# Performance work log

Hardware: AMD Instinct MI355X
Metric: run time of the kernel (lower is better)

## Reference

```python
import jax, jax.numpy as jnp
import numpy as np

HEADS = 16
HEAD_DIM = 64
DIM = 1024
INNER = HEADS * HEAD_DIM
EPS = 1e-5


def setup_inputs() -> dict:
    key = jax.random.key(0)
    k_x, k_qkv, k_out, k_b = jax.random.split(key, 4)
    B, L = 2, 2048
    x = jax.random.normal(k_x, (B, L, DIM), dtype=jnp.float32)
    # Linear weights stored as [in, out] for x @ W
    w_qkv = jax.random.normal(k_qkv, (DIM, 3 * INNER), dtype=jnp.float32) * (DIM ** -0.5)
    w_out = jax.random.normal(k_out, (INNER, DIM), dtype=jnp.float32) * (INNER ** -0.5)
    b_out = jax.random.normal(k_b, (DIM,), dtype=jnp.float32) * 0.02
    gamma = jnp.ones((DIM,), dtype=jnp.float32)
    beta = jnp.zeros((DIM,), dtype=jnp.float32)
    return {"x": x, "w_qkv": w_qkv, "w_out": w_out, "b_out": b_out, "gamma": gamma, "beta": beta}


def reference(x, w_qkv, w_out, b_out, gamma, beta):
    B, L, C = x.shape
    scale = HEAD_DIM ** -0.5
    qkv = x @ w_qkv  # [B, L, 3*INNER]
    q, k, v = jnp.split(qkv, 3, axis=-1)
    # [B, L, INNER] -> [B, H, L, D]
    def split_heads(t):
        return t.reshape(B, L, HEADS, HEAD_DIM).transpose(0, 2, 1, 3)
    q, k, v = split_heads(q), split_heads(k), split_heads(v)
    dots = jnp.einsum('bhid,bhjd->bhij', q, k) * scale
    attn = jax.nn.softmax(dots, axis=-1)
    out = jnp.einsum('bhij,bhjd->bhid', attn, v)
    out = out.transpose(0, 2, 1, 3).reshape(B, L, INNER)
    out = out @ w_out + b_out
    res = x + out
    mean = jnp.mean(res, axis=-1, keepdims=True)
    var = jnp.var(res, axis=-1, keepdims=True)
    return (res - mean) * jax.lax.rsqrt(var + EPS) * gamma + beta
```

## Files before the change

kernel.cpp:

```cpp
#include <hip/hip_runtime.h>
#include <hip/hip_bf16.h>
#include <stdint.h>

#define HEADS 16
#define HDIM  64
#define DIMC  1024
#define INNER 1024
#define LSEQ  2048
#define BLM   4096

typedef unsigned short u16;
typedef __attribute__((ext_vector_type(8))) short bf16x8;
typedef __attribute__((ext_vector_type(4))) float f32x4;

__device__ __forceinline__ u16 f2bf(float f) {
  union { float f; uint32_t u; } v; v.f = f;
  uint32_t u = v.u;
  return (u16)((u + 0x7fffu + ((u >> 16) & 1u)) >> 16);
}
__device__ __forceinline__ uint32_t pack_bf2(float a, float b) {
  float2 f2; f2.x = a; f2.y = b;
  __hip_bfloat162 t = __float22bfloat162_rn(f2);
  union { __hip_bfloat162 h; uint32_t u; } c; c.h = t; return c.u;
}

__device__ __forceinline__ void load_lds16(const void* g, void* l) {
  __builtin_amdgcn_global_load_lds(
      (const __attribute__((address_space(1))) uint32_t*)g,
      (__attribute__((address_space(3))) uint32_t*)l, 16, 0, 0);
}

__global__ __launch_bounds__(256) void cast_bf16_k(const float* __restrict__ in,
                                                   u16* __restrict__ out, int n) {
  int i = (blockIdx.x * 256 + threadIdx.x) * 4;
  if (i < n) {
    float4 v = *(const float4*)(in + i);
    ushort4 o;
    o.x = f2bf(v.x); o.y = f2bf(v.y); o.z = f2bf(v.z); o.w = f2bf(v.w);
    *(ushort4*)(out + i) = o;
  }
}

__global__ __launch_bounds__(256) void transpose_cast_k(const float* __restrict__ in,
                                                        u16* __restrict__ out,
                                                        int R, int C) {
  __shared__ float tile[32][33];
  int c0 = blockIdx.x * 32, r0 = blockIdx.y * 32;
  int j = threadIdx.x & 31, i0 = threadIdx.x >> 5;
#pragma unroll
  for (int p = 0; p < 4; ++p) {
    int i = i0 + p * 8;
    tile[i][j] = in[(size_t)(r0 + i) * C + (c0 + j)];
  }
  __syncthreads();
#pragma unroll
  for (int p = 0; p < 4; ++p) {
    int i = i0 + p * 8;
    out[(size_t)(c0 + i) * R + (r0 + j)] = f2bf(tile[j][i]);
  }
}

template <int EPI>
__global__ __launch_bounds__(256) void gemm_bt(const u16* __restrict__ A,
                                               const u16* __restrict__ Bt,
                                               u16* __restrict__ Cb,
                                               float* __restrict__ Cf,
                                               const float* __restrict__ bias,
                                               const float* __restrict__ resid,
                                               u16* __restrict__ Vt,
                                               int M, int N, int K) {
  __shared__ alignas(16) u16 As[128 * 32];
  __shared__ alignas(16) u16 Bs[128 * 32];
  const int tid = threadIdx.x;
  const int lane = tid & 63;
  const int w = tid >> 6;
  const int wm = w >> 1, wn = w & 1;
  const int m0 = blockIdx.y * 128, n0 = blockIdx.x * 128;
  const int ln = lane & 15, qq = lane >> 4;
  const f32x4 zero4 = {0.f, 0.f, 0.f, 0.f};

  f32x4 acc[4][4];
#pragma unroll
  for (int i = 0; i < 4; ++i)
#pragma unroll
    for (int j = 0; j < 4; ++j) acc[i][j] = zero4;

  for (int kt = 0; kt < K; kt += 32) {
    __syncthreads();
#pragma unroll
    for (int iss = 0; iss < 2; ++iss) {
      int t = iss * 256 + tid;
      int r = t >> 2;
      int cl = (t & 3) ^ ((r >> 1) & 3);
      load_lds16(A + (size_t)(m0 + r) * K + kt + cl * 8,
                 (char*)As + (iss * 256 + w * 64) * 16);
      load_lds16(Bt + (size_t)(n0 + r) * K + kt + cl * 8,
                 (char*)Bs + (iss * 256 + w * 64) * 16);
    }
    __syncthreads();
    bf16x8 af[4], bfr[4];
#pragma unroll
    for (int i = 0; i < 4; ++i) {
      int ra = wm * 64 + i * 16 + ln;
      af[i] = *(const bf16x8*)(As + (ra * 4 + (qq ^ ((ra >> 1) & 3))) * 8);
      int rb = wn * 64 + i * 16 + ln;
      bfr[i] = *(const bf16x8*)(Bs + (rb * 4 + (qq ^ ((rb >> 1) & 3))) * 8);
    }
#pragma unroll
    for (int i = 0; i < 4; ++i)
#pragma unroll
      for (int j = 0; j < 4; ++j)
        acc[i][j] = __builtin_amdgcn_mfma_f32_16x16x32_bf16(af[i], bfr[j],
                                                            acc[i][j], 0, 0, 0);
  }

#pragma unroll
  for (int i = 0; i < 4; ++i) {
#pragma unroll
    for (int j = 0; j < 4; ++j) {
      int col = n0 + wn * 64 + j * 16 + ln;
      if (EPI == 0) {
#pragma unroll
        for (int rr = 0; rr < 4; ++rr) {
          int row = m0 + wm * 64 + i * 16 + qq * 4 + rr;
          Cb[(size_t)row * N + col] = f2bf(acc[i][j][rr]);
        }
      } else if (EPI == 1) {
#pragma unroll
        for (int rr = 0; rr < 4; ++rr) {
          int row = m0 + wm * 64 + i * 16 + qq * 4 + rr;
          Cf[(size_t)row * N + col] =
              acc[i][j][rr] + bias[col] + resid[(size_t)row * N + col];
        }
      } else {
        if (col < 2048) {
#pragma unroll
          for (int rr = 0; rr < 4; ++rr) {
            int row = m0 + wm * 64 + i * 16 + qq * 4 + rr;
            Cb[(size_t)row * 2048 + col] = f2bf(acc[i][j][rr]);
          }
        } else {
          int dg = col - 2048;
          int hh = dg >> 6, dd = dg & 63;
          int l0 = (m0 & 2047) + wm * 64 + i * 16 + qq * 4;
          int bb = m0 >> 11;
          ushort4 pk;
          pk.x = f2bf(acc[i][j][0]); pk.y = f2bf(acc[i][j][1]);
          pk.z = f2bf(acc[i][j][2]); pk.w = f2bf(acc[i][j][3]);
          *(ushort4*)(Vt + (((size_t)bb * 16 + hh) * 64 + dd) * 2048 + l0) = pk;
        }
      }
    }
  }
}

__global__ __launch_bounds__(256) void attn_fused(const u16* __restrict__ qk,
                                                  const u16* __restrict__ vt,
                                                  u16* __restrict__ outp) {
  const int qt = blockIdx.x & 31;
  const int h = (blockIdx.x >> 5) & 15;
  const int b = blockIdx.x >> 9;
  const int tid = threadIdx.x;
  const int lane = tid & 63;
  const int w = tid >> 6;
  const int ln = lane & 15, q4 = lane >> 4;
  const int l7 = ln & 7;
  const f32x4 zero4 = {0.f, 0.f, 0.f, 0.f};

  __shared__ alignas(16) u16 Ks[64 * 64];
  __shared__ alignas(16) u16 Vs[64 * 64];
  __shared__ alignas(16) u16 Ps[4][16 * 72];

  const size_t bh_tok = (size_t)b * LSEQ;
  const size_t vbase = ((size_t)b * 16 + h) * 64 * 2048;
  const int baseQ = h * HDIM;

  bf16x8 qf[2];
  {
    int row = qt * 64 + w * 16 + ln;
    const u16* p = qk + (bh_tok + row) * 2048 + baseQ;
#pragma unroll
    for (int ks = 0; ks < 2; ++ks) {
      bf16x8 v = *(const bf16x8*)(p + q4 * 8 + 32 * ks);
      bf16x8 o;
#pragma unroll
      for (int jj = 0; jj < 8; ++jj) {
        union { uint32_t u; float f; } cv; cv.u = ((uint32_t)(u16)v[jj]) << 16;
        o[jj] = (short)f2bf(cv.f * 0.125f);
      }
      qf[ks] = o;
    }
  }

  float mT = -1e30f, lsum = 0.f;
  f32x4 o_acc[4];
#pragma unroll
  for (int dt = 0; dt < 4; ++dt) o_acc[dt] = zero4;

  u16* pw_base = &Ps[w][0];

  for (int jt = 0; jt < 32; ++jt) {
    const int key0 = jt * 64;
    __syncthreads();
#pragma unroll
    for (int iss = 0; iss < 2; ++iss) {
      int idx = iss * 256 + tid;
      int row = idx >> 3, c = idx & 7;
      int cl = c ^ (row & 7);
      load_lds16(qk + (bh_tok + key0 + row) * 2048 + 1024 + baseQ + cl * 8,
                 (char*)Ks + (iss * 256 + w * 64) * 16);
      load_lds16(vt + vbase + (size_t)row * 2048 + key0 + cl * 8,
                 (char*)Vs + (iss * 256 + w * 64) * 16);
    }
    __syncthreads();

    f32x4 S[4];
#pragma unroll
    for (int kt = 0; kt < 4; ++kt) {
      f32x4 a = zero4;
#pragma unroll
      for (int ks = 0; ks < 2; ++ks) {
        bf16x8 kf = *(const bf16x8*)(
            Ks + (((kt * 16 + ln) * 8 + ((ks * 4 + q4) ^ l7)) * 8));
        a = __builtin_amdgcn_mfma_f32_16x16x32_bf16(kf, qf[ks], a, 0, 0, 0);
      }
      S[kt] = a;
    }

    float mx = S[0][0];
#pragma unroll
    for (int kt = 0; kt < 4; ++kt)
#pragma unroll
      for (int r = 0; r < 4; ++r) mx = fmaxf(mx, S[kt][r]);
    mx = fmaxf(mx, __shfl_xor(mx, 16));
    mx = fmaxf(mx, __shfl_xor(mx, 32));
    float mnew = fmaxf(mT, mx);
    float alpha = __expf(mT - mnew);
    float sl = 0.f;
#pragma unroll
    for (int kt = 0; kt < 4; ++kt)
#pragma unroll
      for (int r = 0; r < 4; ++r) {
        float p = __expf(S[kt][r] - mnew);
        S[kt][r] = p;
        sl += p;
      }
    sl += __shfl_xor(sl, 16);
    sl += __shfl_xor(sl, 32);
    lsum = lsum * alpha + sl;
    mT = mnew;
#pragma unroll
    for (int dt = 0; dt < 4; ++dt) o_acc[dt] *= alpha;

#pragma unroll
    for (int kt = 0; kt < 4; ++kt)
#pragma unroll
      for (int hh = 0; hh < 2; ++hh) {
        uint32_t pd = pack_bf2(S[kt][2 * hh], S[kt][2 * hh + 1]);
        *(uint32_t*)(pw_base + ln * 72 + kt * 16 + q4 * 4 + 2 * hh) = pd;
      }
    asm volatile("s_waitcnt lgkmcnt(0)" ::: "memory");

    bf16x8 pf0 = *(const bf16x8*)(pw_base + ln * 72 + 0 * 32 + q4 * 8);
    bf16x8 pf1 = *(const bf16x8*)(pw_base + ln * 72 + 1 * 32 + q4 * 8);

#pragma unroll
    for (int dt = 0; dt < 4; ++dt) {
      bf16x8 va0 = *(const bf16x8*)(
          Vs + (((dt * 16 + ln) * 8 + ((0 * 4 + q4) ^ l7)) * 8));
      o_acc[dt] = __builtin_amdgcn_mfma_f32_16x16x32_bf16(va0, pf0, o_acc[dt], 0, 0, 0);
      bf16x8 va1 = *(const bf16x8*)(
          Vs + (((dt * 16 + ln) * 8 + ((1 * 4 + q4) ^ l7)) * 8));
      o_acc[dt] = __builtin_amdgcn_mfma_f32_16x16x32_bf16(va1, pf1, o_acc[dt], 0, 0, 0);
    }
  }

  float rl = 1.0f / lsum;
  asm volatile("s_waitcnt lgkmcnt(0)" ::: "memory");
#pragma unroll
  for (int dt = 0; dt < 4; ++dt)
#pragma unroll
    for (int hh = 0; hh < 2; ++hh) {
      uint32_t pd = pack_bf2(o_acc[dt][2 * hh] * rl, o_acc[dt][2 * hh + 1] * rl);
      *(uint32_t*)(pw_base + ln * 72 + dt * 16 + q4 * 4 + 2 * hh) = pd;
    }
  asm volatile("s_waitcnt lgkmcnt(0)" ::: "memory");
#pragma unroll
  for (int half = 0; half < 2; ++half) {
    int rr = half * 8 + (lane >> 3);
    int ch = lane & 7;
    bf16x8 rowv = *(const bf16x8*)(pw_base + rr * 72 + ch * 8);
    int tok = qt * 64 + w * 16 + rr;
    *(bf16x8*)(outp + (bh_tok + tok) * 1024 + baseQ + ch * 8) = rowv;
  }
}

__global__ __launch_bounds__(256) void ln_k(const float* __restrict__ res,
                                            const float* __restrict__ gamma,
                                            const float* __restrict__ beta,
                                            float* __restrict__ out) {
  int row = blockIdx.x;
  const float* r = res + (size_t)row * DIMC;
  int tid = threadIdx.x;
  float4 v = *(const float4*)(r + tid * 4);
  float s = v.x + v.y + v.z + v.w;
  float ss = v.x * v.x + v.y * v.y + v.z * v.z + v.w * v.w;
#pragma unroll
  for (int off = 1; off < 64; off <<= 1) {
    s += __shfl_xor(s, off);
    ss += __shfl_xor(ss, off);
  }
  __shared__ float sbuf[8];
  int w = tid >> 6, lane = tid & 63;
  if (lane == 0) { sbuf[w] = s; sbuf[4 + w] = ss; }
  __syncthreads();
  s = sbuf[0] + sbuf[1] + sbuf[2] + sbuf[3];
  ss = sbuf[4] + sbuf[5] + sbuf[6] + sbuf[7];
  float mean = s * (1.0f / DIMC);
  float var = ss * (1.0f / DIMC) - mean * mean;
  float inv = rsqrtf(var + 1e-5f);
  float4 g = *(const float4*)(gamma + tid * 4);
  float4 bt = *(const float4*)(beta + tid * 4);
  float4 o;
  o.x = (v.x - mean) * inv * g.x + bt.x;
  o.y = (v.y - mean) * inv * g.y + bt.y;
  o.z = (v.z - mean) * inv * g.z + bt.z;
  o.w = (v.w - mean) * inv * g.w + bt.w;
  *(float4*)(out + (size_t)row * DIMC + tid * 4) = o;
}

extern "C" void kernel_launch(void* const* d_in, const int* in_sizes, int n_in,
                              void* d_out, int out_size, void* d_ws, size_t ws_size,
                              hipStream_t stream) {
  const float* x = (const float*)d_in[0];
  const float* w_qkv = (const float*)d_in[1];
  const float* w_out = (const float*)d_in[2];
  const float* b_out = (const float*)d_in[3];
  const float* gamma = (const float*)d_in[4];
  const float* beta = (const float*)d_in[5];
  float* outp = (float*)d_out;
  char* ws = (char*)d_ws;

  u16* xb = (u16*)(ws);
  u16* wqkvT = (u16*)(ws + ((size_t)8 << 20));
  u16* qk = (u16*)(ws + ((size_t)14 << 20));
  u16* vt = (u16*)(ws + ((size_t)30 << 20));
  u16* attnout = (u16*)(ws);
  u16* woutT = (u16*)(ws + ((size_t)8 << 20));
  float* res = (float*)(ws + ((size_t)14 << 20));

  cast_bf16_k<<<4096, 256, 0, stream>>>(x, xb, BLM * DIMC);
  transpose_cast_k<<<dim3(96, 32), 256, 0, stream>>>(w_qkv, wqkvT, 1024, 3072);
  gemm_bt<2><<<dim3(24, 32), 256, 0, stream>>>(xb, wqkvT, qk, nullptr, nullptr,
                                               nullptr, vt, BLM, 3072, 1024);
  transpose_cast_k<<<dim3(32, 32), 256, 0, stream>>>(w_out, woutT, 1024, 1024);
  attn_fused<<<1024, 256, 0, stream>>>(qk, vt, attnout);
  gemm_bt<1><<<dim3(8, 32), 256, 0, stream>>>(attnout, woutT, nullptr, res, b_out,
                                              x, nullptr, BLM, 1024, 1024);
  ln_k<<<4096, 256, 0, stream>>>(res, gamma, beta, outp);
}
```

Measured before the change: 231.3 us.

## Process two query sub-tiles per wave in attention to reuse K/V fragments

Each attention block now handles 128 query rows instead of 64, with every wave owning two 16-row query sub-tiles, so each K and V fragment read from LDS feeds two MFMAs. The grid drops from 1024 to 512 blocks, which halves the global K/V tile traffic per query and the number of LDS fragment reads per MFMA. The cost is more registers for the doubled accumulators and score tiles, and fewer blocks to spread across the 256 CUs, which may lower occupancy and leave some CUs idle.

```diff
diff --git a/kernel.cpp b/kernel.cpp
--- a/kernel.cpp
+++ b/kernel.cpp
@@ -157,9 +157,9 @@
 __global__ __launch_bounds__(256) void attn_fused(const u16* __restrict__ qk,
                                                   const u16* __restrict__ vt,
                                                   u16* __restrict__ outp) {
-  const int qt = blockIdx.x & 31;
-  const int h = (blockIdx.x >> 5) & 15;
-  const int b = blockIdx.x >> 9;
+  const int qt = blockIdx.x & 15;
+  const int h = (blockIdx.x >> 4) & 15;
+  const int b = blockIdx.x >> 8;
   const int tid = threadIdx.x;
   const int lane = tid & 63;
   const int w = tid >> 6;
@@ -169,15 +169,16 @@
 
   __shared__ alignas(16) u16 Ks[64 * 64];
   __shared__ alignas(16) u16 Vs[64 * 64];
-  __shared__ alignas(16) u16 Ps[4][16 * 72];
+  __shared__ alignas(16) u16 Ps[4][32 * 72];
 
   const size_t bh_tok = (size_t)b * LSEQ;
   const size_t vbase = ((size_t)b * 16 + h) * 64 * 2048;
   const int baseQ = h * HDIM;
 
-  bf16x8 qf[2];
-  {
-    int row = qt * 64 + w * 16 + ln;
+  bf16x8 qf[2][2];
+#pragma unroll
+  for (int qi = 0; qi < 2; ++qi) {
+    int row = qt * 128 + w * 32 + qi * 16 + ln;
     const u16* p = qk + (bh_tok + row) * 2048 + baseQ;
 #pragma unroll
     for (int ks = 0; ks < 2; ++ks) {
@@ -188,14 +189,16 @@
         union { uint32_t u; float f; } cv; cv.u = ((uint32_t)(u16)v[jj]) << 16;
         o[jj] = (short)f2bf(cv.f * 0.125f);
       }
-      qf[ks] = o;
-    }
-  }
-
-  float mT = -1e30f, lsum = 0.f;
-  f32x4 o_acc[4];
-#pragma unroll
-  for (int dt = 0; dt < 4; ++dt) o_acc[dt] = zero4;
+      qf[ks][qi] = o;
+    }
+  }
+
+  float mT[2] = {-1e30f, -1e30f}, lsum[2] = {0.f, 0.f};
+  f32x4 o_acc[2][4];
+#pragma unroll
+  for (int qi = 0; qi < 2; ++qi)
+#pragma unroll
+    for (int dt = 0; dt < 4; ++dt) o_acc[qi][dt] = zero4;
 
   u16* pw_base = &Ps[w][0];
 
@@ -214,83 +217,100 @@
     }
     __syncthreads();
 
-    f32x4 S[4];
-#pragma unroll
-    for (int kt = 0; kt < 4; ++kt) {
-      f32x4 a = zero4;
+    f32x4 S2[2][4];
+#pragma unroll
+    for (int qi = 0; qi < 2; ++qi)
+#pragma unroll
+      for (int kt = 0; kt < 4; ++kt) S2[qi][kt] = zero4;
+#pragma unroll
+    for (int kt = 0; kt < 4; ++kt)
 #pragma unroll
       for (int ks = 0; ks < 2; ++ks) {
         bf16x8 kf = *(const bf16x8*)(
             Ks + (((kt * 16 + ln) * 8 + ((ks * 4 + q4) ^ l7)) * 8));
-        a = __builtin_amdgcn_mfma_f32_16x16x32_bf16(kf, qf[ks], a, 0, 0, 0);
-      }
-      S[kt] = a;
-    }
-
-    float mx = S[0][0];
-#pragma unroll
-    for (int kt = 0; kt < 4; ++kt)
-#pragma unroll
-      for (int r = 0; r < 4; ++r) mx = fmaxf(mx, S[kt][r]);
-    mx = fmaxf(mx, __shfl_xor(mx, 16));
-    mx = fmaxf(mx, __shfl_xor(mx, 32));
-    float mnew = fmaxf(mT, mx);
-    float alpha = __expf(mT - mnew);
-    float sl = 0.f;
-#pragma unroll
-    for (int kt = 0; kt < 4; ++kt)
-#pragma unroll
-      for (int r = 0; r < 4; ++r) {
-        float p = __expf(S[kt][r] - mnew);
-        S[kt][r] = p;
-        sl += p;
-      }
-    sl += __shfl_xor(sl, 16);
-    sl += __shfl_xor(sl, 32);
-    lsum = lsum * alpha + sl;
-    mT = mnew;
-#pragma unroll
-    for (int dt = 0; dt < 4; ++dt) o_acc[dt] *= alpha;
-
-#pragma unroll
-    for (int kt = 0; kt < 4; ++kt)
-#pragma unroll
-      for (int hh = 0; hh < 2; ++hh) {
-        uint32_t pd = pack_bf2(S[kt][2 * hh], S[kt][2 * hh + 1]);
-        *(uint32_t*)(pw_base + ln * 72 + kt * 16 + q4 * 4 + 2 * hh) = pd;
-      }
+#pragma unroll
+        for (int qi = 0; qi < 2; ++qi)
+          S2[qi][kt] = __builtin_amdgcn_mfma_f32_16x16x32_bf16(
+              kf, qf[ks][qi], S2[qi][kt], 0, 0, 0);
+      }
+
+#pragma unroll
+    for (int qi = 0; qi < 2; ++qi) {
+      float mx = S2[qi][0][0];
+#pragma unroll
+      for (int kt = 0; kt < 4; ++kt)
+#pragma unroll
+        for (int r = 0; r < 4; ++r) mx = fmaxf(mx, S2[qi][kt][r]);
+      mx = fmaxf(mx, __shfl_xor(mx, 16));
+      mx = fmaxf(mx, __shfl_xor(mx, 32));
+      float mnew = fmaxf(mT[qi], mx);
+      float alpha = __expf(mT[qi] - mnew);
+      float sl = 0.f;
+#pragma unroll
+      for (int kt = 0; kt < 4; ++kt)
+#pragma unroll
+        for (int r = 0; r < 4; ++r) {
+          float p = __expf(S2[qi][kt][r] - mnew);
+          S2[qi][kt][r] = p;
+          sl += p;
+        }
+      sl += __shfl_xor(sl, 16);
+      sl += __shfl_xor(sl, 32);
+      lsum[qi] = lsum[qi] * alpha + sl;
+      mT[qi] = mnew;
+#pragma unroll
+      for (int dt = 0; dt < 4; ++dt) o_acc[qi][dt] *= alpha;
+
+#pragma unroll
+      for (int kt = 0; kt < 4; ++kt) {
+        uint2 pd;
+        pd.x = pack_bf2(S2[qi][kt][0], S2[qi][kt][1]);
+        pd.y = pack_bf2(S2[qi][kt][2], S2[qi][kt][3]);
+        *(uint2*)(pw_base + (qi * 16 + ln) * 72 + kt * 16 + q4 * 4) = pd;
+      }
+    }
     asm volatile("s_waitcnt lgkmcnt(0)" ::: "memory");
 
-    bf16x8 pf0 = *(const bf16x8*)(pw_base + ln * 72 + 0 * 32 + q4 * 8);
-    bf16x8 pf1 = *(const bf16x8*)(pw_base + ln * 72 + 1 * 32 + q4 * 8);
-
+    bf16x8 pf[2][2];
+#pragma unroll
+    for (int qi = 0; qi < 2; ++qi)
+#pragma unroll
+      for (int ks = 0; ks < 2; ++ks)
+        pf[qi][ks] = *(const bf16x8*)(pw_base + (qi * 16 + ln) * 72 + ks * 32 +
+                                      q4 * 8);
+
+#pragma unroll
+    for (int dt = 0; dt < 4; ++dt)
+#pragma unroll
+      for (int ks = 0; ks < 2; ++ks) {
+        bf16x8 va = *(const bf16x8*)(
+            Vs + (((dt * 16 + ln) * 8 + ((ks * 4 + q4) ^ l7)) * 8));
+#pragma unroll
+        for (int qi = 0; qi < 2; ++qi)
+          o_acc[qi][dt] = __builtin_amdgcn_mfma_f32_16x16x32_bf16(
+              va, pf[qi][ks], o_acc[qi][dt], 0, 0, 0);
+      }
+  }
+
+  asm volatile("s_waitcnt lgkmcnt(0)" ::: "memory");
+#pragma unroll
+  for (int qi = 0; qi < 2; ++qi) {
+    float rl = 1.0f / lsum[qi];
 #pragma unroll
     for (int dt = 0; dt < 4; ++dt) {
-      bf16x8 va0 = *(const bf16x8*)(
-          Vs + (((dt * 16 + ln) * 8 + ((0 * 4 + q4) ^ l7)) * 8));
-      o_acc[dt] = __builtin_amdgcn_mfma_f32_16x16x32_bf16(va0, pf0, o_acc[dt], 0, 0, 0);
-      bf16x8 va1 = *(const bf16x8*)(
-          Vs + (((dt * 16 + ln) * 8 + ((1 * 4 + q4) ^ l7)) * 8));
-      o_acc[dt] = __builtin_amdgcn_mfma_f32_16x16x32_bf16(va1, pf1, o_acc[dt], 0, 0, 0);
-    }
-  }
-
-  float rl = 1.0f / lsum;
+      uint2 pd;
+      pd.x = pack_bf2(o_acc[qi][dt][0] * rl, o_acc[qi][dt][1] * rl);
+      pd.y = pack_bf2(o_acc[qi][dt][2] * rl, o_acc[qi][dt][3] * rl);
+      *(uint2*)(pw_base + (qi * 16 + ln) * 72 + dt * 16 + q4 * 4) = pd;
+    }
+  }
   asm volatile("s_waitcnt lgkmcnt(0)" ::: "memory");
 #pragma unroll
-  for (int dt = 0; dt < 4; ++dt)
-#pragma unroll
-    for (int hh = 0; hh < 2; ++hh) {
-      uint32_t pd = pack_bf2(o_acc[dt][2 * hh] * rl, o_acc[dt][2 * hh + 1] * rl);
-      *(uint32_t*)(pw_base + ln * 72 + dt * 16 + q4 * 4 + 2 * hh) = pd;
-    }
-  asm volatile("s_waitcnt lgkmcnt(0)" ::: "memory");
-#pragma unroll
-  for (int half = 0; half < 2; ++half) {
-    int rr = half * 8 + (lane >> 3);
+  for (int pass = 0; pass < 4; ++pass) {
+    int rr = pass * 8 + (lane >> 3);
     int ch = lane & 7;
     bf16x8 rowv = *(const bf16x8*)(pw_base + rr * 72 + ch * 8);
-    int tok = qt * 64 + w * 16 + rr;
+    int tok = qt * 128 + w * 32 + rr;
     *(bf16x8*)(outp + (bh_tok + tok) * 1024 + baseQ + ch * 8) = rowv;
   }
 }
@@ -354,7 +374,7 @@
   gemm_bt<2><<<dim3(24, 32), 256, 0, stream>>>(xb, wqkvT, qk, nullptr, nullptr,
                                                nullptr, vt, BLM, 3072, 1024);
   transpose_cast_k<<<dim3(32, 32), 256, 0, stream>>>(w_out, woutT, 1024, 1024);
-  attn_fused<<<1024, 256, 0, stream>>>(qk, vt, attnout);
+  attn_fused<<<512, 256, 0, stream>>>(qk, vt, attnout);
   gemm_bt<1><<<dim3(8, 32), 256, 0, stream>>>(attnout, woutT, nullptr, res, b_out,
                                               x, nullptr, BLM, 1024, 1024);
   ln_k<<<4096, 256, 0, stream>>>(res, gamma, beta, outp);
```

New measurement: 235.9 us. About the same (+2.0%).
